# Optimization experiments

Hardware: AMD Instinct MI355X
Metric: run time of the kernel (lower is better)

Reference implementation:

```python
import jax, jax.numpy as jnp
import numpy as np

MASK_NUM = float(-2**32 + 1)  # additive masking constant from the original module


def setup_inputs() -> dict:
    key = jax.random.key(0)
    kq, kk, kv, km = jax.random.split(key, 4)
    BH, S, D = 32, 2048, 64   # batch*heads, seq_len, head_dim
    B = 4                     # true batch (masks leading dim)
    queries = jax.random.normal(kq, (BH, S, D), dtype=jnp.float32)
    keys = jax.random.normal(kk, (BH, S, D), dtype=jnp.float32)
    values = jax.random.normal(kv, (BH, S, D), dtype=jnp.float32)
    masks = jax.random.randint(km, (B, S), 0, 2, dtype=jnp.int32)  # 1 = masked key
    return {"queries": queries, "keys": keys, "values": values, "masks": masks}


def reference(queries, keys, values, masks):
    d = queries.shape[-1]
    # QK^T, scaled by sqrt(d): [BH, Sq, Sk]
    scores = jnp.einsum('bqd,bkd->bqk', queries, keys) / (d ** 0.5)
    # key-padding mask: tile [B, Sk] -> [BH, Sk], additive large negative
    heads = queries.shape[0] // masks.shape[0]
    m = jnp.tile(masks.astype(jnp.float32), (heads, 1))[:, None, :]  # [BH,1,Sk]
    scores = scores + m * MASK_NUM
    # causal (future) mask: replace upper-triangular entries with MASK_NUM
    Sq, Sk = scores.shape[1], scores.shape[2]
    tril = jnp.tril(jnp.ones((Sq, Sk), dtype=scores.dtype))
    scores = jnp.where(tril == 0, MASK_NUM, scores)
    attn = jax.nn.softmax(scores, axis=-1)
    # dropout_rate = 0.0 -> identity
    return jnp.einsum('bqk,bkd->bqd', attn, values)
```

## Files before the change

### kernel.cpp

```cpp
#include <hip/hip_runtime.h>
#include <hip/hip_bf16.h>

#define S_LEN  2048
#define DHEAD  64
#define NHEADS 32
#define NBATCH 4
#define LOG2E  1.44269504f
#define CMASK  (-4294967296.0f * 1.44269504f)

typedef __attribute__((ext_vector_type(4)))  float f4;
typedef __attribute__((ext_vector_type(8)))  short bh8;
typedef __attribute__((ext_vector_type(16))) float f16x;
typedef __attribute__((ext_vector_type(4)))  int   i4;
typedef unsigned short ushort_t;

static __device__ __forceinline__ unsigned short f2b(float f){
    unsigned int x = __builtin_bit_cast(unsigned int, f);
    x += 0x7FFFu + ((x >> 16) & 1u);
    return (unsigned short)(x >> 16);
}
static __device__ __forceinline__ float b2f(ushort_t u){
    return __builtin_bit_cast(float, ((unsigned)u) << 16);
}
static __device__ __forceinline__ int cvtpk(float a, float b){
    int r; asm("v_cvt_pk_bf16_f32 %0, %1, %2" : "=v"(r) : "v"(a), "v"(b)); return r;
}

__global__ __launch_bounds__(256)
void prep(const float* __restrict__ K, const float* __restrict__ V,
          const int* __restrict__ M,
          ushort_t* __restrict__ Kb, ushort_t* __restrict__ Vt,
          float* __restrict__ colpart, unsigned* __restrict__ mbits)
{
    const int bid = blockIdx.x;
    const int tid = threadIdx.x;
    if (bid < 2048){
        const int i = bid * 256 + tid;
        const f4* p = (const f4*)(K + (size_t)i * 8);
        f4 a = p[0], b = p[1];
        bh8 w;
        #pragma unroll
        for (int k = 0; k < 4; ++k){ w[k] = (short)f2b(a[k]); w[k+4] = (short)f2b(b[k]); }
        *(bh8*)(Kb + (size_t)i * 8) = w;
    } else if (bid < 3072){
        __shared__ short T[64][72];
        __shared__ float red[64][4];
        const int r2 = bid - 2048;
        const int head = r2 >> 5;
        const int kv0  = (r2 & 31) * 64;
        {
            const int r = tid >> 2;
            const int s = (tid & 3) * 16;
            const float* vp = V + ((size_t)head * S_LEN + kv0 + r) * DHEAD + s;
            f4 v0 = *(const f4*)(vp);
            f4 v1 = *(const f4*)(vp + 4);
            f4 v2 = *(const f4*)(vp + 8);
            f4 v3 = *(const f4*)(vp + 12);
            float vv[16];
            *(f4*)&vv[0] = v0; *(f4*)&vv[4] = v1; *(f4*)&vv[8] = v2; *(f4*)&vv[12] = v3;
            #pragma unroll
            for (int i = 0; i < 16; ++i) T[r][s + i] = (short)f2b(vv[i]);
        }
        __syncthreads();
        {
            const int d  = tid >> 2;
            const int k0 = (tid & 3) * 16;
            bh8 w0, w1;
            float s16 = 0.f;
            #pragma unroll
            for (int i = 0; i < 8; ++i){
                w0[i] = T[k0 + i][d];
                w1[i] = T[k0 + 8 + i][d];
                s16 += b2f((ushort_t)w0[i]) + b2f((ushort_t)w1[i]);
            }
            ushort_t* op = Vt + ((size_t)head * DHEAD + d) * S_LEN + kv0 + k0;
            *(bh8*)op       = w0;
            *(bh8*)(op + 8) = w1;
            red[d][tid & 3] = s16;
        }
        __syncthreads();
        if (tid < 64)
            colpart[(size_t)r2 * 64 + tid] =
                red[tid][0] + red[tid][1] + red[tid][2] + red[tid][3];
    } else {
        const int* mp = M + ((size_t)(tid >> 6) << 11) + ((tid & 63) << 5);
        unsigned bits = 0u;
        #pragma unroll
        for (int j = 0; j < 32; j += 4){
            i4 v = *(const i4*)(mp + j);
            bits |= (v[0] != 0 ? (1u << j) : 0u) | (v[1] != 0 ? (2u << j) : 0u)
                  | (v[2] != 0 ? (4u << j) : 0u) | (v[3] != 0 ? (8u << j) : 0u);
        }
        mbits[tid] = bits;
    }
}

__global__ __launch_bounds__(256, 2)
void attn_main(const float* __restrict__ Q, const ushort_t* __restrict__ Kb,
               const ushort_t* __restrict__ Vt, const unsigned* __restrict__ mbits,
               float* __restrict__ Out)
{
    __shared__ char SMEM[2][16384];

    const int tid  = threadIdx.x;
    const int wave = tid >> 6;
    const int lane = tid & 63;
    const int lq   = lane & 31;
    const int hi   = lane >> 5;

    const int bid  = blockIdx.x;
    const int head = ((bid & 7) << 2) | ((bid >> 3) & 3);
    const int a    = bid >> 5;
    const int j    = (a < 8) ? (15 - a) : (a - 8);
    const int b    = head & (NBATCH - 1);
    const size_t hoff = (size_t)head * S_LEN * DHEAD;

    const int q0w = (j << 7) + (wave << 5);
    const int dq  = q0w + lq;
    const int td  = q0w >> 6;
    const int nt  = (j << 1) + 2;

    const ushort_t* kbase = Kb + hoff;
    const ushort_t* vbase = Vt + (size_t)head * DHEAD * S_LEN;

    const int mwords = __builtin_bit_cast(int, mbits[(b << 6) + lane]);

    bh8 qB[4];
    {
        const float* qp = Q + hoff + (size_t)(q0w + lq) * DHEAD;
        const float qs = 0.125f * LOG2E;
        #pragma unroll
        for (int ks = 0; ks < 4; ++ks){
            f4 f0 = *(const f4*)(qp + ks * 16 + hi * 8);
            f4 f1 = *(const f4*)(qp + ks * 16 + hi * 8 + 4);
            bh8 aa;
            #pragma unroll
            for (int i = 0; i < 4; ++i){
                aa[i]   = (short)f2b(f0[i] * qs);
                aa[i+4] = (short)f2b(f1[i] * qs);
            }
            qB[ks] = aa;
        }
    }

    auto stage = [&](int buf, int kv0){
        #pragma unroll
        for (int i = 0; i < 2; ++i){
            const int o   = ((i << 8) + tid) << 4;
            const int row = o >> 7;
            const int cb  = (o & 127) ^ ((row & 7) << 4);
            const char* ks = (const char*)kbase + (size_t)(kv0 + row) * 128 + cb;
            const char* vs = (const char*)vbase + (size_t)row * (S_LEN * 2)
                             + (size_t)kv0 * 2 + cb;
            __builtin_amdgcn_global_load_lds(
                (const __attribute__((address_space(1))) void*)ks,
                (__attribute__((address_space(3))) void*)(&SMEM[buf][o]), 16, 0, 0);
            __builtin_amdgcn_global_load_lds(
                (const __attribute__((address_space(1))) void*)vs,
                (__attribute__((address_space(3))) void*)(&SMEM[buf][8192 + o]), 16, 0, 0);
        }
    };

    f16x acc0 = {};
    f16x acc1 = {};
    float m = -INFINITY, l = 0.f;

    stage(0, 0);
    asm volatile("s_waitcnt vmcnt(0)" ::: "memory");
    __syncthreads();

    for (int t = 0; t < nt; ++t){
        const int cur = t & 1;
        if (t + 1 < nt) stage(cur ^ 1, (t + 1) << 6);

        if (t <= td){
            const int kv0 = t << 6;
            const char* kb = &SMEM[cur][0];
            const char* vb = &SMEM[cur][8192];

            bh8 kf[8];
            #pragma unroll
            for (int t32 = 0; t32 < 2; ++t32)
                #pragma unroll
                for (int ks = 0; ks < 4; ++ks){
                    const int rl = (t32 << 5) + lq;
                    const int cb = ((ks << 5) + (hi << 4)) ^ ((rl & 7) << 4);
                    kf[t32*4+ks] = *(const bh8*)(kb + (rl << 7) + cb);
                }

            f16x s0 = {}, s1 = {};
            __builtin_amdgcn_s_setprio(1);
            #pragma unroll
            for (int ks = 0; ks < 4; ++ks)
                s0 = __builtin_amdgcn_mfma_f32_32x32x16_bf16(kf[ks],   qB[ks], s0, 0, 0, 0);
            #pragma unroll
            for (int ks = 0; ks < 4; ++ks)
                s1 = __builtin_amdgcn_mfma_f32_32x32x16_bf16(kf[4+ks], qB[ks], s1, 0, 0, 0);
            __builtin_amdgcn_s_setprio(0);

            bh8 vf[8];
            #pragma unroll
            for (int aa = 0; aa < 2; ++aa)
                #pragma unroll
                for (int j4 = 0; j4 < 4; ++j4){
                    const int rl = (aa << 5) + lq;
                    const int cb = ((j4 << 5) + (hi << 4)) ^ ((rl & 7) << 4);
                    vf[aa*4+j4] = *(const bh8*)(vb + (rl << 7) + cb);
                }

            const unsigned ml0 = ((unsigned)__builtin_amdgcn_readlane(mwords, 2*t    )) >> (hi << 2);
            const unsigned ml1 = ((unsigned)__builtin_amdgcn_readlane(mwords, 2*t + 1)) >> (hi << 2);
            #pragma unroll
            for (int g = 0; g < 4; ++g)
                #pragma unroll
                for (int i = 0; i < 4; ++i){
                    s0[g*4+i] = ((ml0 >> (g*8+i)) & 1u) ? CMASK : s0[g*4+i];
                    s1[g*4+i] = ((ml1 >> (g*8+i)) & 1u) ? CMASK : s1[g*4+i];
                }
            if (t == td){
                #pragma unroll
                for (int g = 0; g < 4; ++g)
                    #pragma unroll
                    for (int i = 0; i < 4; ++i){
                        const int k0i = kv0 + (g << 3) + (hi << 2) + i;
                        s0[g*4+i] = (k0i      > dq) ? CMASK : s0[g*4+i];
                        s1[g*4+i] = (k0i + 32 > dq) ? CMASK : s1[g*4+i];
                    }
            }

            float t8[8];
            #pragma unroll
            for (int i = 0; i < 8; ++i)
                t8[i] = fmaxf(fmaxf(s0[i], s0[i+8]), fmaxf(s1[i], s1[i+8]));
            #pragma unroll
            for (int i = 0; i < 4; ++i) t8[i] = fmaxf(t8[i], t8[i+4]);
            float pml = fmaxf(fmaxf(t8[0], t8[1]), fmaxf(t8[2], t8[3]));
            float pm  = fmaxf(pml, __shfl_xor(pml, 32, 64));

            if (!__all(pm <= m + 11.0f)){
                float mn = fmaxf(m, pm);
                float al = __builtin_amdgcn_exp2f(m - mn);
                m = mn;
                l *= al;
                #pragma unroll
                for (int i = 0; i < 16; ++i){ acc0[i] *= al; acc1[i] *= al; }
            }

            #pragma unroll
            for (int i = 0; i < 16; ++i){
                s0[i] = __builtin_amdgcn_exp2f(s0[i] - m);
                s1[i] = __builtin_amdgcn_exp2f(s1[i] - m);
            }
            float u8[8];
            #pragma unroll
            for (int i = 0; i < 8; ++i) u8[i] = (s0[i] + s0[i+8]) + (s1[i] + s1[i+8]);
            #pragma unroll
            for (int i = 0; i < 4; ++i) u8[i] = u8[i] + u8[i+4];
            float lsl = (u8[0] + u8[1]) + (u8[2] + u8[3]);
            l += lsl + __shfl_xor(lsl, 32, 64);

            bh8 pa[4];
            #pragma unroll
            for (int half = 0; half < 2; ++half){
                const f16x& sv = half ? s1 : s0;
                int D[8];
                #pragma unroll
                for (int g = 0; g < 4; ++g){
                    D[2*g]   = cvtpk(sv[4*g],   sv[4*g+1]);
                    D[2*g+1] = cvtpk(sv[4*g+2], sv[4*g+3]);
                }
                int sA0 = hi ? D[0] : D[2],  sA1 = hi ? D[1] : D[3];
                int sB0 = hi ? D[4] : D[6],  sB1 = hi ? D[5] : D[7];
                int rA0 = __shfl_xor(sA0, 32, 64), rA1 = __shfl_xor(sA1, 32, 64);
                int rB0 = __shfl_xor(sB0, 32, 64), rB1 = __shfl_xor(sB1, 32, 64);
                i4 p0 = { hi ? rA0 : D[0], hi ? rA1 : D[1],
                          hi ? D[2] : rA0, hi ? D[3] : rA1 };
                i4 p1 = { hi ? rB0 : D[4], hi ? rB1 : D[5],
                          hi ? D[6] : rB0, hi ? D[7] : rB1 };
                pa[half*2]     = __builtin_bit_cast(bh8, p0);
                pa[half*2 + 1] = __builtin_bit_cast(bh8, p1);
            }

            __builtin_amdgcn_s_setprio(1);
            #pragma unroll
            for (int j4 = 0; j4 < 4; ++j4){
                acc0 = __builtin_amdgcn_mfma_f32_32x32x16_bf16(vf[j4],   pa[j4], acc0, 0, 0, 0);
                acc1 = __builtin_amdgcn_mfma_f32_32x32x16_bf16(vf[4+j4], pa[j4], acc1, 0, 0, 0);
            }
            __builtin_amdgcn_s_setprio(0);
        }

        asm volatile("s_waitcnt vmcnt(0)" ::: "memory");
        __syncthreads();
    }

    const float inv = 1.0f / l;
    float* op = Out + hoff + (size_t)(q0w + lq) * DHEAD;
    #pragma unroll
    for (int g = 0; g < 4; ++g){
        f4 o0, o1;
        #pragma unroll
        for (int i = 0; i < 4; ++i){
            o0[i] = acc0[g * 4 + i] * inv;
            o1[i] = acc1[g * 4 + i] * inv;
        }
        *(f4*)(op + g * 8 + hi * 4)      = o0;
        *(f4*)(op + 32 + g * 8 + hi * 4) = o1;
    }
}

__global__ __launch_bounds__(256)
void attn_fixup(const float* __restrict__ colpart, const int* __restrict__ M,
                float* __restrict__ Out)
{
    __shared__ float red[4][64];
    __shared__ int qstar;
    const int head = blockIdx.x;
    const int b = head & (NBATCH - 1);
    const int tid = threadIdx.x;
    const int col = tid & 63;
    const int grp = tid >> 6;
    {
        float s = 0.f;
        const float* cp = colpart + ((size_t)head * 32 + grp * 8) * 64 + col;
        #pragma unroll
        for (int j = 0; j < 8; ++j) s += cp[j * 64];
        red[grp][col] = s;
    }
    if (tid == 0){
        int q = 0;
        const int* mp = M + (size_t)b * S_LEN;
        while (q < S_LEN && mp[q]) ++q;
        qstar = q;
    }
    __syncthreads();
    const int qs = qstar;
    if (qs == 0) return;
    const float mean = (red[0][col] + red[1][col] + red[2][col] + red[3][col])
                       * (1.0f / S_LEN);
    for (int q = grp; q < qs; q += 4)
        Out[((size_t)head * S_LEN + q) * DHEAD + col] = mean;
}

extern "C" void kernel_launch(void* const* d_in, const int* in_sizes, int n_in,
                              void* d_out, int out_size, void* d_ws, size_t ws_size,
                              hipStream_t stream)
{
    const float* Q = (const float*)d_in[0];
    const float* K = (const float*)d_in[1];
    const float* V = (const float*)d_in[2];
    const int*   M = (const int*)d_in[3];
    float* Out = (float*)d_out;

    ushort_t* Kb = (ushort_t*)d_ws;
    ushort_t* Vt = Kb + (size_t)NHEADS * S_LEN * DHEAD;
    float* colpart = (float*)(Vt + (size_t)NHEADS * S_LEN * DHEAD);
    unsigned* mbits = (unsigned*)(colpart + 1024 * 64);

    prep      <<<dim3(3073),   dim3(256), 0, stream>>>(K, V, M, Kb, Vt, colpart, mbits);
    attn_main <<<dim3(512),    dim3(256), 0, stream>>>(Q, Kb, Vt, mbits, Out);
    attn_fixup<<<dim3(NHEADS), dim3(256), 0, stream>>>(colpart, M, Out);
}
```

Measured before the change: 69.84 us.

## Split KV range into two halves per query tile and merge partials

Each query tile's causal KV range is split into two halves, each handled by its own block, so attn_main now launches 1024 blocks. Each block writes an unnormalised bf16 partial output plus its running max and sum. A new attn_merge kernel rescales and combines the two partials into the final fp32 output. The aim is better load balance and a shorter critical path per block. In exchange it adds an extra launch, extra global traffic for the partial buffers, and rounds the partial accumulators to bf16.

```diff
diff --git a/kernel.cpp b/kernel.cpp
--- a/kernel.cpp
+++ b/kernel.cpp
@@ -12,6 +12,7 @@
 typedef __attribute__((ext_vector_type(8)))  short bh8;
 typedef __attribute__((ext_vector_type(16))) float f16x;
 typedef __attribute__((ext_vector_type(4)))  int   i4;
+typedef __attribute__((ext_vector_type(2)))  int   i2;
 typedef unsigned short ushort_t;
 
 static __device__ __forceinline__ unsigned short f2b(float f){
@@ -98,7 +99,7 @@
 __global__ __launch_bounds__(256, 2)
 void attn_main(const float* __restrict__ Q, const ushort_t* __restrict__ Kb,
                const ushort_t* __restrict__ Vt, const unsigned* __restrict__ mbits,
-               float* __restrict__ Out)
+               ushort_t* __restrict__ Obuf, float* __restrict__ mlbuf)
 {
     __shared__ char SMEM[2][16384];
 
@@ -110,15 +111,17 @@
 
     const int bid  = blockIdx.x;
     const int head = ((bid & 7) << 2) | ((bid >> 3) & 3);
-    const int a    = bid >> 5;
-    const int j    = (a < 8) ? (15 - a) : (a - 8);
+    const int c    = bid >> 5;
+    const int s    = c & 1;
+    const int j    = 15 - (c >> 1);
     const int b    = head & (NBATCH - 1);
     const size_t hoff = (size_t)head * S_LEN * DHEAD;
 
     const int q0w = (j << 7) + (wave << 5);
     const int dq  = q0w + lq;
     const int td  = q0w >> 6;
-    const int nt  = (j << 1) + 2;
+    const int kt0 = s * (j + 1);
+    const int ntb = j + 1;
 
     const ushort_t* kbase = Kb + hoff;
     const ushort_t* vbase = Vt + (size_t)head * DHEAD * S_LEN;
@@ -165,16 +168,17 @@
     f16x acc1 = {};
     float m = -INFINITY, l = 0.f;
 
-    stage(0, 0);
+    stage(0, kt0 << 6);
     asm volatile("s_waitcnt vmcnt(0)" ::: "memory");
     __syncthreads();
 
-    for (int t = 0; t < nt; ++t){
-        const int cur = t & 1;
-        if (t + 1 < nt) stage(cur ^ 1, (t + 1) << 6);
-
-        if (t <= td){
-            const int kv0 = t << 6;
+    for (int i = 0; i < ntb; ++i){
+        const int cur = i & 1;
+        const int kt  = kt0 + i;
+        if (i + 1 < ntb) stage(cur ^ 1, (kt + 1) << 6);
+
+        if (kt <= td){
+            const int kv0 = kt << 6;
             const char* kb = &SMEM[cur][0];
             const char* vb = &SMEM[cur][8192];
 
@@ -208,32 +212,32 @@
                     vf[aa*4+j4] = *(const bh8*)(vb + (rl << 7) + cb);
                 }
 
-            const unsigned ml0 = ((unsigned)__builtin_amdgcn_readlane(mwords, 2*t    )) >> (hi << 2);
-            const unsigned ml1 = ((unsigned)__builtin_amdgcn_readlane(mwords, 2*t + 1)) >> (hi << 2);
+            const unsigned ml0 = ((unsigned)__builtin_amdgcn_readlane(mwords, 2*kt    )) >> (hi << 2);
+            const unsigned ml1 = ((unsigned)__builtin_amdgcn_readlane(mwords, 2*kt + 1)) >> (hi << 2);
             #pragma unroll
             for (int g = 0; g < 4; ++g)
                 #pragma unroll
-                for (int i = 0; i < 4; ++i){
-                    s0[g*4+i] = ((ml0 >> (g*8+i)) & 1u) ? CMASK : s0[g*4+i];
-                    s1[g*4+i] = ((ml1 >> (g*8+i)) & 1u) ? CMASK : s1[g*4+i];
+                for (int i2_ = 0; i2_ < 4; ++i2_){
+                    s0[g*4+i2_] = ((ml0 >> (g*8+i2_)) & 1u) ? CMASK : s0[g*4+i2_];
+                    s1[g*4+i2_] = ((ml1 >> (g*8+i2_)) & 1u) ? CMASK : s1[g*4+i2_];
                 }
-            if (t == td){
+            if (kt == td){
                 #pragma unroll
                 for (int g = 0; g < 4; ++g)
                     #pragma unroll
-                    for (int i = 0; i < 4; ++i){
-                        const int k0i = kv0 + (g << 3) + (hi << 2) + i;
-                        s0[g*4+i] = (k0i      > dq) ? CMASK : s0[g*4+i];
-                        s1[g*4+i] = (k0i + 32 > dq) ? CMASK : s1[g*4+i];
+                    for (int i2_ = 0; i2_ < 4; ++i2_){
+                        const int k0i = kv0 + (g << 3) + (hi << 2) + i2_;
+                        s0[g*4+i2_] = (k0i      > dq) ? CMASK : s0[g*4+i2_];
+                        s1[g*4+i2_] = (k0i + 32 > dq) ? CMASK : s1[g*4+i2_];
                     }
             }
 
             float t8[8];
             #pragma unroll
-            for (int i = 0; i < 8; ++i)
-                t8[i] = fmaxf(fmaxf(s0[i], s0[i+8]), fmaxf(s1[i], s1[i+8]));
-            #pragma unroll
-            for (int i = 0; i < 4; ++i) t8[i] = fmaxf(t8[i], t8[i+4]);
+            for (int i2_ = 0; i2_ < 8; ++i2_)
+                t8[i2_] = fmaxf(fmaxf(s0[i2_], s0[i2_+8]), fmaxf(s1[i2_], s1[i2_+8]));
+            #pragma unroll
+            for (int i2_ = 0; i2_ < 4; ++i2_) t8[i2_] = fmaxf(t8[i2_], t8[i2_+4]);
             float pml = fmaxf(fmaxf(t8[0], t8[1]), fmaxf(t8[2], t8[3]));
             float pm  = fmaxf(pml, __shfl_xor(pml, 32, 64));
 
@@ -243,19 +247,19 @@
                 m = mn;
                 l *= al;
                 #pragma unroll
-                for (int i = 0; i < 16; ++i){ acc0[i] *= al; acc1[i] *= al; }
-            }
-
-            #pragma unroll
-            for (int i = 0; i < 16; ++i){
-                s0[i] = __builtin_amdgcn_exp2f(s0[i] - m);
-                s1[i] = __builtin_amdgcn_exp2f(s1[i] - m);
+                for (int i2_ = 0; i2_ < 16; ++i2_){ acc0[i2_] *= al; acc1[i2_] *= al; }
+            }
+
+            #pragma unroll
+            for (int i2_ = 0; i2_ < 16; ++i2_){
+                s0[i2_] = __builtin_amdgcn_exp2f(s0[i2_] - m);
+                s1[i2_] = __builtin_amdgcn_exp2f(s1[i2_] - m);
             }
             float u8[8];
             #pragma unroll
-            for (int i = 0; i < 8; ++i) u8[i] = (s0[i] + s0[i+8]) + (s1[i] + s1[i+8]);
-            #pragma unroll
-            for (int i = 0; i < 4; ++i) u8[i] = u8[i] + u8[i+4];
+            for (int i2_ = 0; i2_ < 8; ++i2_) u8[i2_] = (s0[i2_] + s0[i2_+8]) + (s1[i2_] + s1[i2_+8]);
+            #pragma unroll
+            for (int i2_ = 0; i2_ < 4; ++i2_) u8[i2_] = u8[i2_] + u8[i2_+4];
             float lsl = (u8[0] + u8[1]) + (u8[2] + u8[3]);
             l += lsl + __shfl_xor(lsl, 32, 64);
 
@@ -294,18 +298,48 @@
         __syncthreads();
     }
 
-    const float inv = 1.0f / l;
-    float* op = Out + hoff + (size_t)(q0w + lq) * DHEAD;
+    ushort_t* ob = Obuf + (((size_t)(s * NHEADS + head) * S_LEN + q0w + lq) << 6);
     #pragma unroll
     for (int g = 0; g < 4; ++g){
-        f4 o0, o1;
-        #pragma unroll
-        for (int i = 0; i < 4; ++i){
-            o0[i] = acc0[g * 4 + i] * inv;
-            o1[i] = acc1[g * 4 + i] * inv;
-        }
-        *(f4*)(op + g * 8 + hi * 4)      = o0;
-        *(f4*)(op + 32 + g * 8 + hi * 4) = o1;
+        i2 w0, w1;
+        w0[0] = cvtpk(acc0[4*g],   acc0[4*g+1]);
+        w0[1] = cvtpk(acc0[4*g+2], acc0[4*g+3]);
+        w1[0] = cvtpk(acc1[4*g],   acc1[4*g+1]);
+        w1[1] = cvtpk(acc1[4*g+2], acc1[4*g+3]);
+        *(i2*)((char*)ob + 16*g + 8*hi)      = w0;
+        *(i2*)((char*)ob + 64 + 16*g + 8*hi) = w1;
+    }
+    if (hi == 0){
+        float* mlp = mlbuf + (((size_t)(s * NHEADS + head) * S_LEN + q0w + lq) << 1);
+        mlp[0] = m;
+        mlp[1] = l;
+    }
+}
+
+__global__ __launch_bounds__(256)
+void attn_merge(const ushort_t* __restrict__ Obuf, const float* __restrict__ mlbuf,
+                float* __restrict__ Out)
+{
+    const int gid  = blockIdx.x * 256 + threadIdx.x;
+    const int row  = gid >> 2;
+    const int part = gid & 3;
+    const float* ml0 = mlbuf + ((size_t)row << 1);
+    const float* ml1 = mlbuf + (((size_t)(NHEADS * S_LEN) + row) << 1);
+    const float m0 = ml0[0], l0 = ml0[1];
+    const float m1 = ml1[0], l1 = ml1[1];
+    const float ms = fmaxf(m0, m1);
+    const float a0 = __builtin_amdgcn_exp2f(m0 - ms);
+    const float a1 = __builtin_amdgcn_exp2f(m1 - ms);
+    const float inv = 1.0f / (a0 * l0 + a1 * l1);
+    const ushort_t* o0 = Obuf + ((size_t)row << 6) + part * 16;
+    const ushort_t* o1 = o0 + ((size_t)(NHEADS * S_LEN) << 6);
+    bh8 x0a = *(const bh8*)(o0), x0b = *(const bh8*)(o0 + 8);
+    bh8 x1a = *(const bh8*)(o1), x1b = *(const bh8*)(o1 + 8);
+    float* op = Out + ((size_t)row << 6) + part * 16;
+    #pragma unroll
+    for (int i = 0; i < 8; ++i){
+        op[i]     = (a0 * b2f((ushort_t)x0a[i]) + a1 * b2f((ushort_t)x1a[i])) * inv;
+        op[8 + i] = (a0 * b2f((ushort_t)x0b[i]) + a1 * b2f((ushort_t)x1b[i])) * inv;
     }
 }
 
@@ -356,8 +390,11 @@
     ushort_t* Vt = Kb + (size_t)NHEADS * S_LEN * DHEAD;
     float* colpart = (float*)(Vt + (size_t)NHEADS * S_LEN * DHEAD);
     unsigned* mbits = (unsigned*)(colpart + 1024 * 64);
+    ushort_t* Obuf = (ushort_t*)(mbits + 256);
+    float* mlbuf = (float*)(Obuf + ((size_t)2 * NHEADS * S_LEN * DHEAD));
 
     prep      <<<dim3(3073),   dim3(256), 0, stream>>>(K, V, M, Kb, Vt, colpart, mbits);
-    attn_main <<<dim3(512),    dim3(256), 0, stream>>>(Q, Kb, Vt, mbits, Out);
+    attn_main <<<dim3(1024),   dim3(256), 0, stream>>>(Q, Kb, Vt, mbits, Obuf, mlbuf);
+    attn_merge<<<dim3(1024),   dim3(256), 0, stream>>>(Obuf, mlbuf, Out);
     attn_fixup<<<dim3(NHEADS), dim3(256), 0, stream>>>(colpart, M, Out);
 }
```

After: 64.89 us. -7.1%, faster.
